# Optimization experiments

Measured on AMD Instinct MI355X. Metric: run time of the kernel, lower is better.

Reference implementation:

```python
import jax, jax.numpy as jnp
import numpy as np

N = 50000      # num_nodes
E = 800000     # num_edges (before self loops)
EMB = 128      # emb_dim
GH = 64        # gcn_hidden
TD = 4         # temporal_dim
B = 64         # batch of sequences
T = 200        # max sequence length
H = 128        # lstm_hidden (per direction)
IN_DIM = 2 + EMB + TD


def lstm_scan(x_tbi, w_ih, w_hh, b_ih, b_hh):
    """x_tbi: [T, B, I] -> hidden states [T, B, H]. PyTorch gate order i,f,g,o."""
    Bsz = x_tbi.shape[1]
    Hh = w_hh.shape[1]

    def step(carry, xt):
        h, c = carry
        g = xt @ w_ih.T + h @ w_hh.T + b_ih + b_hh
        i, f, gg, o = jnp.split(g, 4, axis=-1)
        c = jax.nn.sigmoid(f) * c + jax.nn.sigmoid(i) * jnp.tanh(gg)
        h = jax.nn.sigmoid(o) * jnp.tanh(c)
        return (h, c), h

    init = (jnp.zeros((Bsz, Hh), x_tbi.dtype), jnp.zeros((Bsz, Hh), x_tbi.dtype))
    _, hs = jax.lax.scan(step, init, x_tbi)
    return hs


def gcn_layer(x, W, b, src, dst, ew):
    """PyG GCNConv: linear -> symmetric-norm gather/scatter-add -> bias.
    (self loops already appended to src/dst/ew by caller)"""
    h = x @ W  # [N, out]
    deg = jax.ops.segment_sum(ew, dst, num_segments=N)
    dinv = jnp.where(deg > 0, jax.lax.rsqrt(deg), 0.0)
    norm = dinv[src] * ew * dinv[dst]            # [E+N]
    msg = h[src] * norm[:, None]                  # gather + scale
    return jax.ops.segment_sum(msg, dst, num_segments=N) + b


def setup_inputs() -> dict:
    key = jax.random.key(0)
    ks = jax.random.split(key, 16)
    s = 0.02
    return {
        'x_coords': jax.random.normal(ks[0], (N, 2), jnp.float32),
        'temporal_features': jax.random.uniform(ks[1], (N, TD), jnp.float32, -1.0, 1.0),
        'edge_index': jax.random.randint(ks[2], (2, E), 0, N),
        'edge_weight': jnp.ones((E,), jnp.float32),
        'seq': jax.random.randint(ks[3], (B, T), 0, N),
        'lengths': jax.random.randint(ks[4], (B,), 1, T + 1),
        'node_emb': jax.random.normal(ks[5], (N, EMB), jnp.float32) * s,
        'gcn1_w': jax.random.normal(ks[6], (IN_DIM, GH), jnp.float32) * s,
        'gcn1_b': jnp.zeros((GH,), jnp.float32),
        'gcn2_w': jax.random.normal(ks[7], (GH, EMB), jnp.float32) * s,
        'gcn2_b': jnp.zeros((EMB,), jnp.float32),
        'w_ih_f': jax.random.normal(ks[8], (4 * H, EMB), jnp.float32) * s,
        'w_hh_f': jax.random.normal(ks[9], (4 * H, H), jnp.float32) * s,
        'b_ih_f': jnp.zeros((4 * H,), jnp.float32),
        'b_hh_f': jnp.zeros((4 * H,), jnp.float32),
        'w_ih_b': jax.random.normal(ks[10], (4 * H, EMB), jnp.float32) * s,
        'w_hh_b': jax.random.normal(ks[11], (4 * H, H), jnp.float32) * s,
        'b_ih_b': jnp.zeros((4 * H,), jnp.float32),
        'b_hh_b': jnp.zeros((4 * H,), jnp.float32),
        'attn_w': jax.random.normal(ks[12], (2 * H,), jnp.float32) * s,
        'attn_b': jnp.zeros((), jnp.float32),
        'fc_w': jax.random.normal(ks[13], (2 * H, N), jnp.float32) * s,
        'fc_b': jnp.zeros((N,), jnp.float32),
    }


def reference(x_coords, temporal_features, edge_index, edge_weight, seq, lengths,
              node_emb, gcn1_w, gcn1_b, gcn2_w, gcn2_b,
              w_ih_f, w_hh_f, b_ih_f, b_hh_f,
              w_ih_b, w_hh_b, b_ih_b, b_hh_b,
              attn_w, attn_b, fc_w, fc_b):
    # --- GCN with self loops (PyG add_self_loops=True, fill_value=1) ---
    loop = jnp.arange(N)
    src = jnp.concatenate([edge_index[0], loop])
    dst = jnp.concatenate([edge_index[1], loop])
    ew = jnp.concatenate([edge_weight, jnp.ones((N,), edge_weight.dtype)])

    x = jnp.concatenate([x_coords, node_emb, temporal_features], axis=1)  # [N, 134]
    z = jax.nn.relu(gcn_layer(x, gcn1_w, gcn1_b, src, dst, ew))
    z = gcn_layer(z, gcn2_w, gcn2_b, src, dst, ew)  # dropout = identity (eval)

    # --- sequence embedding + BiLSTM ---
    seq_emb = z[seq]                                  # [B, T, EMB]
    h_f = lstm_scan(seq_emb.transpose(1, 0, 2), w_ih_f, w_hh_f, b_ih_f, b_hh_f)
    h_f = h_f.transpose(1, 0, 2)                      # [B, T, H]

    # backward direction: reverse each sequence within its valid length
    t = jnp.arange(T)
    valid = t[None, :] < lengths[:, None]             # [B, T]
    rev_idx = jnp.where(valid, lengths[:, None] - 1 - t[None, :], t[None, :])
    x_rev = jnp.take_along_axis(seq_emb, rev_idx[:, :, None], axis=1)
    h_b = lstm_scan(x_rev.transpose(1, 0, 2), w_ih_b, w_hh_b, b_ih_b, b_hh_b)
    h_b = jnp.take_along_axis(h_b.transpose(1, 0, 2), rev_idx[:, :, None], axis=1)

    lstm_out = jnp.concatenate([h_f, h_b], axis=-1)   # [B, T, 2H]

    # --- masked attention pooling ---
    scores = lstm_out @ attn_w + attn_b               # [B, T]
    scores = jnp.where(valid, scores, -jnp.inf)
    aw = jax.nn.softmax(scores, axis=1)
    context = jnp.einsum('bt,btd->bd', aw, lstm_out)  # [B, 2H]

    return context @ fc_w + fc_b                      # [B, N]
```

## Files before the change

### kernel.cpp

```cpp
#include <hip/hip_runtime.h>
#include <math.h>

#define NN 50000
#define NE 800000
#define EMB 128
#define GH 64
#define BB 64
#define TT 200
#define HH 128
#define G4 512
#define IND 134
#define PM 128
#define PO 128

__device__ __forceinline__ float sigf(float x) { return 1.0f / (1.0f + __expf(-x)); }
__device__ __forceinline__ float tanhf_(float x) { return 1.0f - 2.0f / (__expf(2.0f * x) + 1.0f); }
__device__ __forceinline__ void fma4(float4& a, float s, const float4 w) {
    a.x += s * w.x; a.y += s * w.y; a.z += s * w.z; a.w += s * w.w;
}

__global__ void hist_kernel(const int* __restrict__ ei, const float* __restrict__ ew,
                            int* __restrict__ cnt, float* __restrict__ degw) {
    int e = blockIdx.x * 256 + threadIdx.x;
    if (e >= NE) return;
    int d = ei[NE + e];
    atomicAdd(&cnt[d], 1);
    atomicAdd(&degw[d], ew[e]);
}

__global__ void dinv_kernel(const float* __restrict__ degw, float* __restrict__ dinv) {
    int n = blockIdx.x * 256 + threadIdx.x;
    if (n >= NN) return;
    dinv[n] = rsqrtf(degw[n] + 1.0f);
}

__global__ __launch_bounds__(1024) void scan1_kernel(const int* __restrict__ cnt,
                                                     int* __restrict__ rs, int* __restrict__ partials) {
    __shared__ int s[1024];
    int gid = blockIdx.x * 1024 + threadIdx.x;
    int v = (gid < NN) ? cnt[gid] : 0;
    s[threadIdx.x] = v;
    __syncthreads();
    for (int off = 1; off < 1024; off <<= 1) {
        int add = (threadIdx.x >= (unsigned)off) ? s[threadIdx.x - off] : 0;
        __syncthreads();
        s[threadIdx.x] += add;
        __syncthreads();
    }
    if (gid < NN) rs[gid] = s[threadIdx.x] - v;
    if (threadIdx.x == 1023) partials[blockIdx.x] = s[1023];
}

__global__ void scan2_kernel(int* __restrict__ partials, int nblk) {
    if (threadIdx.x == 0) {
        int acc = 0;
        for (int i = 0; i < nblk; ++i) { int v = partials[i]; partials[i] = acc; acc += v; }
    }
}

__global__ __launch_bounds__(1024) void scan3_kernel(const int* __restrict__ partials,
                                                     int* __restrict__ rs, int* __restrict__ cursor) {
    int gid = blockIdx.x * 1024 + threadIdx.x;
    if (gid < NN) {
        int v = rs[gid] + partials[gid >> 10];
        rs[gid] = v;
        cursor[gid] = v;
    }
    if (gid == 0) rs[NN] = NE;
}

__global__ void fill_kernel(const int* __restrict__ ei, const float* __restrict__ ew,
                            const float* __restrict__ dinv, int* __restrict__ cursor,
                            int* __restrict__ ssrc, float* __restrict__ sw) {
    int e = blockIdx.x * 256 + threadIdx.x;
    if (e >= NE) return;
    int s = ei[e], d = ei[NE + e];
    int pos = atomicAdd(&cursor[d], 1);
    ssrc[pos] = s;
    sw[pos] = ew[e] * dinv[s] * dinv[d];
}

__global__ __launch_bounds__(256) void gemm1_kernel(const float* __restrict__ coords,
                                                    const float* __restrict__ temporal,
                                                    const float* __restrict__ emb,
                                                    const float* __restrict__ W1,
                                                    float* __restrict__ h1) {
    __shared__ __align__(16) float wl[IND][GH];
    for (int i = threadIdx.x; i < IND * GH / 4; i += 256)
        ((float4*)wl)[i] = ((const float4*)W1)[i];
    __syncthreads();
    int n = blockIdx.x * 256 + threadIdx.x;
    if (n >= NN) return;
    float4 acc[16];
    float c0 = coords[2 * n], c1 = coords[2 * n + 1];
#pragma unroll
    for (int j = 0; j < 16; ++j) {
        float4 wa = *(const float4*)&wl[0][j * 4];
        float4 wb = *(const float4*)&wl[1][j * 4];
        float4 a;
        a.x = c0 * wa.x + c1 * wb.x; a.y = c0 * wa.y + c1 * wb.y;
        a.z = c0 * wa.z + c1 * wb.z; a.w = c0 * wa.w + c1 * wb.w;
        acc[j] = a;
    }
    const float4* er = (const float4*)(emb + (size_t)n * EMB);
#pragma unroll 2
    for (int k4 = 0; k4 < 32; ++k4) {
        float4 v = er[k4];
        int k = 2 + k4 * 4;
#pragma unroll
        for (int j = 0; j < 16; ++j) {
            fma4(acc[j], v.x, *(const float4*)&wl[k][j * 4]);
            fma4(acc[j], v.y, *(const float4*)&wl[k + 1][j * 4]);
            fma4(acc[j], v.z, *(const float4*)&wl[k + 2][j * 4]);
            fma4(acc[j], v.w, *(const float4*)&wl[k + 3][j * 4]);
        }
    }
    float t0 = temporal[4 * n], t1 = temporal[4 * n + 1], t2 = temporal[4 * n + 2], t3 = temporal[4 * n + 3];
#pragma unroll
    for (int j = 0; j < 16; ++j) {
        fma4(acc[j], t0, *(const float4*)&wl[130][j * 4]);
        fma4(acc[j], t1, *(const float4*)&wl[131][j * 4]);
        fma4(acc[j], t2, *(const float4*)&wl[132][j * 4]);
        fma4(acc[j], t3, *(const float4*)&wl[133][j * 4]);
        *(float4*)&h1[(size_t)n * GH + j * 4] = acc[j];
    }
}

__global__ __launch_bounds__(256) void agg_kernel(const float* __restrict__ hin,
                                                  const int* __restrict__ rs,
                                                  const int* __restrict__ ssrc,
                                                  const float* __restrict__ sw,
                                                  const float* __restrict__ dinv,
                                                  const float* __restrict__ bias, int relu,
                                                  float* __restrict__ hout) {
    int lane = threadIdx.x & 63;
    int wid = threadIdx.x >> 6;
    int n = blockIdx.x * 4 + wid;
    if (n >= NN) return;
    float dv = dinv[n];
    float acc = hin[(size_t)n * GH + lane] * (dv * dv);
    int i = rs[n], e1 = rs[n + 1];
    for (; i + 3 < e1; i += 4) {
        int s0 = ssrc[i], s1 = ssrc[i + 1], s2 = ssrc[i + 2], s3 = ssrc[i + 3];
        float w0 = sw[i], w1 = sw[i + 1], w2 = sw[i + 2], w3 = sw[i + 3];
        float a0 = hin[(size_t)s0 * GH + lane];
        float a1 = hin[(size_t)s1 * GH + lane];
        float a2 = hin[(size_t)s2 * GH + lane];
        float a3 = hin[(size_t)s3 * GH + lane];
        acc += a0 * w0 + a1 * w1 + a2 * w2 + a3 * w3;
    }
    for (; i < e1; ++i) acc += hin[(size_t)ssrc[i] * GH + lane] * sw[i];
    if (bias) acc += bias[lane];
    if (relu) acc = fmaxf(acc, 0.0f);
    hout[(size_t)n * GH + lane] = acc;
}

__global__ __launch_bounds__(256) void gemm2_kernel(const float* __restrict__ a2,
                                                    const float* __restrict__ W2,
                                                    const float* __restrict__ b2,
                                                    float* __restrict__ z2) {
    __shared__ __align__(16) float wl[GH][64];
    int j0 = blockIdx.y * 64;
    for (int i = threadIdx.x; i < GH * 16; i += 256) {
        int k = i >> 4, j4 = i & 15;
        *(float4*)&wl[k][j4 * 4] = *(const float4*)&W2[(size_t)k * EMB + j0 + j4 * 4];
    }
    __syncthreads();
    int n = blockIdx.x * 256 + threadIdx.x;
    if (n >= NN) return;
    float4 acc[16];
#pragma unroll
    for (int j = 0; j < 16; ++j) acc[j] = *(const float4*)&b2[j0 + j * 4];
    const float4* ar = (const float4*)(a2 + (size_t)n * GH);
#pragma unroll 2
    for (int k4 = 0; k4 < 16; ++k4) {
        float4 v = ar[k4];
        int k = k4 * 4;
#pragma unroll
        for (int j = 0; j < 16; ++j) {
            fma4(acc[j], v.x, *(const float4*)&wl[k][j * 4]);
            fma4(acc[j], v.y, *(const float4*)&wl[k + 1][j * 4]);
            fma4(acc[j], v.z, *(const float4*)&wl[k + 2][j * 4]);
            fma4(acc[j], v.w, *(const float4*)&wl[k + 3][j * 4]);
        }
    }
#pragma unroll
    for (int j = 0; j < 16; ++j)
        *(float4*)&z2[(size_t)n * EMB + j0 + j * 4] = acc[j];
}

__global__ void gather_kernel(const int* __restrict__ seq, const float* __restrict__ z2,
                              float* __restrict__ se) {
    int idx = blockIdx.x * 256 + threadIdx.x;
    if (idx >= BB * TT * 32) return;
    int r = idx >> 5, q = idx & 31;
    int node = seq[r];
    ((float4*)se)[(size_t)r * 32 + q] = ((const float4*)z2)[(size_t)node * 32 + q];
}

__global__ __launch_bounds__(256) void pregemm_kernel(const float* __restrict__ se,
                                                      const float* __restrict__ w_ih_f,
                                                      const float* __restrict__ w_ih_b,
                                                      const float* __restrict__ b_ih_f,
                                                      const float* __restrict__ b_hh_f,
                                                      const float* __restrict__ b_ih_b,
                                                      const float* __restrict__ b_hh_b,
                                                      const int* __restrict__ lengths,
                                                      float* __restrict__ xpf,
                                                      float* __restrict__ xpb) {
    int dir = blockIdx.z;
    const float* w_ih = dir ? w_ih_b : w_ih_f;
    int o0 = blockIdx.y * PO;
    int m0 = blockIdx.x * PM;
    __shared__ __align__(16) float xs[PM][EMB];
    __shared__ __align__(16) float ws[PO][EMB];
    __shared__ float bsh[PO];
    int tid = threadIdx.x;
#pragma unroll
    for (int i = 0; i < 16; ++i) {
        int idx = i * 256 + tid;
        int row = idx >> 5, c4 = idx & 31;
        float4 v = *(const float4*)&w_ih[(size_t)(o0 + row) * EMB + c4 * 4];
        *(float4*)&ws[row][(c4 ^ ((row >> 3) & 7)) * 4] = v;
    }
    if (tid < PO) bsh[tid] = dir ? (b_ih_b[o0 + tid] + b_hh_b[o0 + tid])
                                 : (b_ih_f[o0 + tid] + b_hh_f[o0 + tid]);
#pragma unroll
    for (int i = 0; i < 16; ++i) {
        int idx = i * 256 + tid;
        int r = idx >> 5, c4 = idx & 31;
        int m = m0 + r;
        int t = m >> 6, b = m & 63;
        int tsrc = t;
        if (dir) { int len = lengths[b]; tsrc = (t < len) ? (len - 1 - t) : t; }
        float4 v = *(const float4*)&se[((size_t)b * TT + tsrc) * EMB + c4 * 4];
        *(float4*)&xs[r][(c4 ^ ((r >> 3) & 3)) * 4] = v;
    }
    __syncthreads();
    int mt = tid >> 4, ot = tid & 15;
    int mswz = mt & 3, oswz = ot & 7;
    float acc[8][8];
#pragma unroll
    for (int mi = 0; mi < 8; ++mi)
#pragma unroll
        for (int oi = 0; oi < 8; ++oi) acc[mi][oi] = 0.0f;
    for (int k4 = 0; k4 < 32; ++k4) {
        int xk = (k4 ^ mswz) * 4;
        int wk = (k4 ^ oswz) * 4;
        float4 xv[8], wv[8];
#pragma unroll
        for (int mi = 0; mi < 8; ++mi) xv[mi] = *(const float4*)&xs[mt * 8 + mi][xk];
#pragma unroll
        for (int oi = 0; oi < 8; ++oi) wv[oi] = *(const float4*)&ws[ot * 8 + oi][wk];
#pragma unroll
        for (int mi = 0; mi < 8; ++mi)
#pragma unroll
            for (int oi = 0; oi < 8; ++oi)
                acc[mi][oi] += xv[mi].x * wv[oi].x + xv[mi].y * wv[oi].y
                             + xv[mi].z * wv[oi].z + xv[mi].w * wv[oi].w;
    }
    float* xp = dir ? xpb : xpf;
#pragma unroll
    for (int mi = 0; mi < 8; ++mi) {
        int m = m0 + mt * 8 + mi;
        int ob = ot * 8;
        float4 oa = make_float4(acc[mi][0] + bsh[ob + 0], acc[mi][1] + bsh[ob + 1],
                                acc[mi][2] + bsh[ob + 2], acc[mi][3] + bsh[ob + 3]);
        float4 obv = make_float4(acc[mi][4] + bsh[ob + 4], acc[mi][5] + bsh[ob + 5],
                                 acc[mi][6] + bsh[ob + 6], acc[mi][7] + bsh[ob + 7]);
        *(float4*)&xp[(size_t)m * G4 + o0 + ob] = oa;
        *(float4*)&xp[(size_t)m * G4 + o0 + ob + 4] = obv;
    }
}

__global__ __launch_bounds__(1024, 4) void lstm_kernel(const float* __restrict__ xpf,
                                                       const float* __restrict__ xpb,
                                                       const float* __restrict__ w_hh_f,
                                                       const float* __restrict__ w_hh_b,
                                                       const int* __restrict__ lengths,
                                                       float* __restrict__ hfo,
                                                       float* __restrict__ hbo) {
    int chain = blockIdx.x;
    int dir = chain & 1, b = chain >> 1;
    const float* w_hh = dir ? w_hh_b : w_hh_f;
    const float* xp = dir ? xpb : xpf;
    float* ho = dir ? hbo : hfo;
    int tid = threadIdx.x;
    int u = tid & 127;
    int kq = tid >> 7;
    int len = lengths[b];

    float4 W[4][4];
#pragma unroll
    for (int g = 0; g < 4; ++g)
#pragma unroll
        for (int j4 = 0; j4 < 4; ++j4)
            W[g][j4] = *(const float4*)&w_hh[(size_t)(g * HH + u) * HH + kq * 16 + j4 * 4];

    __shared__ __align__(16) float hl[HH];
    __shared__ __align__(16) float part[HH][9][4];
    if (tid < HH) hl[tid] = 0.0f;
    __syncthreads();

    float cst = 0.0f;
    float x0 = 0.f, x1 = 0.f, x2 = 0.f, x3 = 0.f;
    const float* xpt = xp + (size_t)b * G4 + u;
    if (tid < HH && len > 0) {
        x0 = xpt[0]; x1 = xpt[HH]; x2 = xpt[2 * HH]; x3 = xpt[3 * HH];
    }
    for (int t = 0; t < len; ++t) {
        const float4* h4 = (const float4*)&hl[kq * 16];
        float a0 = 0.f, a1 = 0.f, a2 = 0.f, a3 = 0.f;
#pragma unroll
        for (int j4 = 0; j4 < 4; ++j4) {
            float4 hv = h4[j4];
            a0 += W[0][j4].x * hv.x + W[0][j4].y * hv.y + W[0][j4].z * hv.z + W[0][j4].w * hv.w;
            a1 += W[1][j4].x * hv.x + W[1][j4].y * hv.y + W[1][j4].z * hv.z + W[1][j4].w * hv.w;
            a2 += W[2][j4].x * hv.x + W[2][j4].y * hv.y + W[2][j4].z * hv.z + W[2][j4].w * hv.w;
            a3 += W[3][j4].x * hv.x + W[3][j4].y * hv.y + W[3][j4].z * hv.z + W[3][j4].w * hv.w;
        }
        *(float4*)&part[u][kq][0] = make_float4(a0, a1, a2, a3);
        __syncthreads();
        if (tid < HH) {
            float n0 = 0.f, n1 = 0.f, n2 = 0.f, n3 = 0.f;
            if (t + 1 < len) {
                const float* xn = xpt + (size_t)(t + 1) * (BB * G4);
                n0 = xn[0]; n1 = xn[HH]; n2 = xn[2 * HH]; n3 = xn[3 * HH];
            }
            float s0 = x0, s1 = x1, s2 = x2, s3 = x3;
#pragma unroll
            for (int q = 0; q < 8; ++q) {
                float4 p = *(const float4*)&part[u][q][0];
                s0 += p.x; s1 += p.y; s2 += p.z; s3 += p.w;
            }
            float gi = sigf(s0), gf = sigf(s1), gg = tanhf_(s2), go = sigf(s3);
            cst = gf * cst + gi * gg;
            float h = go * tanhf_(cst);
            hl[u] = h;
            int tt = dir ? (len - 1 - t) : t;
            ho[((size_t)b * TT + tt) * HH + u] = h;
            x0 = n0; x1 = n1; x2 = n2; x3 = n3;
        }
        __syncthreads();
    }
}

__global__ __launch_bounds__(256) void attn_kernel(const float* __restrict__ hf,
                                                   const float* __restrict__ hb,
                                                   const float* __restrict__ attn_w,
                                                   const float* __restrict__ attn_b,
                                                   const int* __restrict__ lengths,
                                                   float* __restrict__ ctx) {
    int b = blockIdx.x;
    int tid = threadIdx.x;
    int len = lengths[b];
    __shared__ __align__(16) float wl[256];
    __shared__ float pl[256];
    __shared__ float red[256];
    wl[tid] = attn_w[tid];
    __syncthreads();
    float sc = -3.0e38f;
    if (tid < len) {
        const float4* rf = (const float4*)(hf + ((size_t)b * TT + tid) * HH);
        const float4* rb = (const float4*)(hb + ((size_t)b * TT + tid) * HH);
        const float4* w4 = (const float4*)wl;
        float s = attn_b[0];
        for (int k4 = 0; k4 < 32; ++k4) {
            float4 a = rf[k4], ww = w4[k4];
            s += a.x * ww.x + a.y * ww.y + a.z * ww.z + a.w * ww.w;
        }
        for (int k4 = 0; k4 < 32; ++k4) {
            float4 a = rb[k4], ww = w4[32 + k4];
            s += a.x * ww.x + a.y * ww.y + a.z * ww.z + a.w * ww.w;
        }
        sc = s;
    }
    red[tid] = sc;
    __syncthreads();
    for (int off = 128; off > 0; off >>= 1) {
        if (tid < off) red[tid] = fmaxf(red[tid], red[tid + off]);
        __syncthreads();
    }
    float mx = red[0];
    __syncthreads();
    float e = (tid < len) ? __expf(sc - mx) : 0.0f;
    red[tid] = e;
    __syncthreads();
    for (int off = 128; off > 0; off >>= 1) {
        if (tid < off) red[tid] += red[tid + off];
        __syncthreads();
    }
    float inv = 1.0f / red[0];
    pl[tid] = e * inv;
    __syncthreads();
    float acc = 0.0f;
    const float* basep = (tid < HH) ? (hf + (size_t)b * TT * HH + tid)
                                    : (hb + (size_t)b * TT * HH + (tid - HH));
#pragma unroll 4
    for (int t = 0; t < len; ++t) acc += pl[t] * basep[(size_t)t * HH];
    ctx[(size_t)b * 256 + tid] = acc;
}

__global__ __launch_bounds__(256) void fc_kernel(const float* __restrict__ ctx,
                                                 const float* __restrict__ fc_w,
                                                 const float* __restrict__ fc_b,
                                                 float* __restrict__ out) {
    __shared__ __align__(16) float cl[64][256];
    for (int i = threadIdx.x; i < 64 * 256 / 4; i += 256)
        ((float4*)cl)[i] = ((const float4*)ctx)[i];
    __syncthreads();
    int nb = threadIdx.x & 63;
    int bq = threadIdx.x >> 6;
    int n = blockIdx.x * 64 + nb;
    if (n >= NN) return;
    float acc[16];
#pragma unroll
    for (int i = 0; i < 16; ++i) acc[i] = 0.0f;
#pragma unroll 2
    for (int k4 = 0; k4 < 64; ++k4) {
        int k = k4 * 4;
        float w0 = fc_w[(size_t)k * NN + n];
        float w1 = fc_w[(size_t)(k + 1) * NN + n];
        float w2 = fc_w[(size_t)(k + 2) * NN + n];
        float w3 = fc_w[(size_t)(k + 3) * NN + n];
#pragma unroll
        for (int i = 0; i < 16; ++i) {
            float4 cv = *(const float4*)&cl[bq * 16 + i][k];
            acc[i] += cv.x * w0 + cv.y * w1 + cv.z * w2 + cv.w * w3;
        }
    }
    float fb = fc_b[n];
#pragma unroll
    for (int i = 0; i < 16; ++i)
        out[(size_t)(bq * 16 + i) * NN + n] = acc[i] + fb;
}

extern "C" void kernel_launch(void* const* d_in, const int* in_sizes, int n_in,
                              void* d_out, int out_size, void* d_ws, size_t ws_size,
                              hipStream_t stream) {
    const float* x_coords   = (const float*)d_in[0];
    const float* temporal   = (const float*)d_in[1];
    const int*   edge_index = (const int*)d_in[2];
    const float* edge_w     = (const float*)d_in[3];
    const int*   seq        = (const int*)d_in[4];
    const int*   lengths    = (const int*)d_in[5];
    const float* node_emb   = (const float*)d_in[6];
    const float* gcn1_w     = (const float*)d_in[7];
    const float* gcn1_b     = (const float*)d_in[8];
    const float* gcn2_w     = (const float*)d_in[9];
    const float* gcn2_b     = (const float*)d_in[10];
    const float* w_ih_f     = (const float*)d_in[11];
    const float* w_hh_f     = (const float*)d_in[12];
    const float* b_ih_f     = (const float*)d_in[13];
    const float* b_hh_f     = (const float*)d_in[14];
    const float* w_ih_b     = (const float*)d_in[15];
    const float* w_hh_b     = (const float*)d_in[16];
    const float* b_ih_b     = (const float*)d_in[17];
    const float* b_hh_b     = (const float*)d_in[18];
    const float* attn_w     = (const float*)d_in[19];
    const float* attn_b     = (const float*)d_in[20];
    const float* fc_w       = (const float*)d_in[21];
    const float* fc_b       = (const float*)d_in[22];
    float* out = (float*)d_out;

    char* base = (char*)d_ws;
    size_t off = 0;
    auto alloc = [&](size_t nbytes) -> void* {
        void* p = base + off;
        off = (off + nbytes + 255) & ~(size_t)255;
        return p;
    };
    int*   cnt     = (int*)alloc((size_t)2 * NN * 4);
    float* degw    = (float*)(cnt + NN);
    float* dinv    = (float*)alloc((size_t)NN * 4);
    int*   rs      = (int*)alloc(((size_t)NN + 1) * 4);
    int*   cursor  = (int*)alloc((size_t)NN * 4);
    int*   partials= (int*)alloc(64 * 4);
    int*   ssrc    = (int*)alloc((size_t)NE * 4);
    float* sw      = (float*)alloc((size_t)NE * 4);
    float* h1      = (float*)alloc((size_t)NN * GH * 4);
    float* z1      = (float*)alloc((size_t)NN * GH * 4);
    float* a2      = h1;
    float* z2      = (float*)alloc((size_t)NN * EMB * 4);
    float* se      = (float*)alloc((size_t)BB * TT * EMB * 4);
    float* xpf     = (float*)alloc((size_t)TT * BB * G4 * 4);
    float* xpb     = (float*)alloc((size_t)TT * BB * G4 * 4);
    float* hfo     = (float*)alloc((size_t)BB * TT * HH * 4);
    float* hbo     = (float*)alloc((size_t)BB * TT * HH * 4);
    float* ctx     = (float*)alloc((size_t)BB * 256 * 4);
    (void)ws_size; (void)in_sizes; (void)n_in; (void)out_size;

    hipMemsetAsync(cnt, 0, (size_t)2 * NN * 4, stream);

    hist_kernel<<<(NE + 255) / 256, 256, 0, stream>>>(edge_index, edge_w, cnt, degw);
    dinv_kernel<<<(NN + 255) / 256, 256, 0, stream>>>(degw, dinv);
    const int nblk = (NN + 1023) / 1024;
    scan1_kernel<<<nblk, 1024, 0, stream>>>(cnt, rs, partials);
    scan2_kernel<<<1, 64, 0, stream>>>(partials, nblk);
    scan3_kernel<<<nblk, 1024, 0, stream>>>(partials, rs, cursor);
    fill_kernel<<<(NE + 255) / 256, 256, 0, stream>>>(edge_index, edge_w, dinv, cursor, ssrc, sw);

    gemm1_kernel<<<(NN + 255) / 256, 256, 0, stream>>>(x_coords, temporal, node_emb, gcn1_w, h1);
    agg_kernel<<<(NN + 3) / 4, 256, 0, stream>>>(h1, rs, ssrc, sw, dinv, gcn1_b, 1, z1);
    agg_kernel<<<(NN + 3) / 4, 256, 0, stream>>>(z1, rs, ssrc, sw, dinv, (const float*)nullptr, 0, a2);
    gemm2_kernel<<<dim3((NN + 255) / 256, 2), 256, 0, stream>>>(a2, gcn2_w, gcn2_b, z2);

    gather_kernel<<<(BB * TT * 32 + 255) / 256, 256, 0, stream>>>(seq, z2, se);
    pregemm_kernel<<<dim3(TT * BB / PM, G4 / PO, 2), 256, 0, stream>>>(
        se, w_ih_f, w_ih_b, b_ih_f, b_hh_f, b_ih_b, b_hh_b, lengths, xpf, xpb);
    lstm_kernel<<<BB * 2, 1024, 0, stream>>>(xpf, xpb, w_hh_f, w_hh_b, lengths, hfo, hbo);
    attn_kernel<<<BB, 256, 0, stream>>>(hfo, hbo, attn_w, attn_b, lengths, ctx);
    fc_kernel<<<(NN + 63) / 64, 256, 0, stream>>>(ctx, fc_w, fc_b, out);
}
```

Before: 642.3 us.

## Use wave shuffles and double-buffered hidden state in LSTM; register-tile gemm2

The LSTM recurrence now places the 8 k-slices of each hidden unit in adjacent lanes of one wavefront and reduces the gate partials with xor shuffles. This replaces the shared partial array and one of two block barriers per timestep, and the hidden state is double-buffered in padded shared memory. Separately, the second GCN GEMM is rewritten as a 128x64 shared-memory tile with 4x8 register blocking and swizzled layout, using a pre-transposed weight from a new small kernel. Risks are shuffle overhead and one extra kernel launch.

```diff
diff --git a/kernel.cpp b/kernel.cpp
--- a/kernel.cpp
+++ b/kernel.cpp
@@ -155,38 +155,73 @@
     hout[(size_t)n * GH + lane] = acc;
 }
 
+__global__ void w2t_kernel(const float* __restrict__ W2, float* __restrict__ w2t) {
+    int i = blockIdx.x * 256 + threadIdx.x;
+    if (i >= GH * EMB) return;
+    int o = i >> 6, k = i & 63;
+    w2t[i] = W2[(size_t)k * EMB + o];
+}
+
 __global__ __launch_bounds__(256) void gemm2_kernel(const float* __restrict__ a2,
-                                                    const float* __restrict__ W2,
+                                                    const float* __restrict__ w2t,
                                                     const float* __restrict__ b2,
                                                     float* __restrict__ z2) {
-    __shared__ __align__(16) float wl[GH][64];
-    int j0 = blockIdx.y * 64;
-    for (int i = threadIdx.x; i < GH * 16; i += 256) {
-        int k = i >> 4, j4 = i & 15;
-        *(float4*)&wl[k][j4 * 4] = *(const float4*)&W2[(size_t)k * EMB + j0 + j4 * 4];
-    }
-    __syncthreads();
-    int n = blockIdx.x * 256 + threadIdx.x;
-    if (n >= NN) return;
-    float4 acc[16];
-#pragma unroll
-    for (int j = 0; j < 16; ++j) acc[j] = *(const float4*)&b2[j0 + j * 4];
-    const float4* ar = (const float4*)(a2 + (size_t)n * GH);
-#pragma unroll 2
+    int m0 = blockIdx.x * 128, o0 = blockIdx.y * 64;
+    __shared__ __align__(16) float xs[128][64];
+    __shared__ __align__(16) float wt[64][64];
+    __shared__ float bsh[64];
+    int tid = threadIdx.x;
+#pragma unroll
+    for (int i = 0; i < 8; ++i) {
+        int idx = i * 256 + tid;
+        int r = idx >> 4, c4 = idx & 15;
+        int m = m0 + r;
+        float4 v = (m < NN) ? *(const float4*)&a2[(size_t)m * GH + c4 * 4]
+                            : make_float4(0.f, 0.f, 0.f, 0.f);
+        *(float4*)&xs[r][(c4 ^ ((r >> 2) & 3)) * 4] = v;
+    }
+#pragma unroll
+    for (int i = 0; i < 4; ++i) {
+        int idx = i * 256 + tid;
+        int r = idx >> 4, c4 = idx & 15;
+        float4 v = *(const float4*)&w2t[(size_t)(o0 + r) * GH + c4 * 4];
+        *(float4*)&wt[r][(c4 ^ ((r >> 3) & 7)) * 4] = v;
+    }
+    if (tid < 64) bsh[tid] = b2[o0 + tid];
+    __syncthreads();
+    int mt = tid >> 3, ot = tid & 7;
+    float acc[4][8];
+#pragma unroll
+    for (int mi = 0; mi < 4; ++mi)
+#pragma unroll
+        for (int oi = 0; oi < 8; ++oi) acc[mi][oi] = 0.0f;
     for (int k4 = 0; k4 < 16; ++k4) {
-        float4 v = ar[k4];
-        int k = k4 * 4;
-#pragma unroll
-        for (int j = 0; j < 16; ++j) {
-            fma4(acc[j], v.x, *(const float4*)&wl[k][j * 4]);
-            fma4(acc[j], v.y, *(const float4*)&wl[k + 1][j * 4]);
-            fma4(acc[j], v.z, *(const float4*)&wl[k + 2][j * 4]);
-            fma4(acc[j], v.w, *(const float4*)&wl[k + 3][j * 4]);
-        }
-    }
-#pragma unroll
-    for (int j = 0; j < 16; ++j)
-        *(float4*)&z2[(size_t)n * EMB + j0 + j * 4] = acc[j];
+        int xc = (k4 ^ (mt & 3)) * 4;
+        int wc = (k4 ^ (ot & 7)) * 4;
+        float4 xv[4], wv[8];
+#pragma unroll
+        for (int mi = 0; mi < 4; ++mi) xv[mi] = *(const float4*)&xs[mt * 4 + mi][xc];
+#pragma unroll
+        for (int oi = 0; oi < 8; ++oi) wv[oi] = *(const float4*)&wt[ot * 8 + oi][wc];
+#pragma unroll
+        for (int mi = 0; mi < 4; ++mi)
+#pragma unroll
+            for (int oi = 0; oi < 8; ++oi)
+                acc[mi][oi] += xv[mi].x * wv[oi].x + xv[mi].y * wv[oi].y
+                             + xv[mi].z * wv[oi].z + xv[mi].w * wv[oi].w;
+    }
+#pragma unroll
+    for (int mi = 0; mi < 4; ++mi) {
+        int m = m0 + mt * 4 + mi;
+        if (m >= NN) continue;
+        int ob = ot * 8;
+        float4 oa = make_float4(acc[mi][0] + bsh[ob + 0], acc[mi][1] + bsh[ob + 1],
+                                acc[mi][2] + bsh[ob + 2], acc[mi][3] + bsh[ob + 3]);
+        float4 obv = make_float4(acc[mi][4] + bsh[ob + 4], acc[mi][5] + bsh[ob + 5],
+                                 acc[mi][6] + bsh[ob + 6], acc[mi][7] + bsh[ob + 7]);
+        *(float4*)&z2[(size_t)m * EMB + o0 + ob] = oa;
+        *(float4*)&z2[(size_t)m * EMB + o0 + ob + 4] = obv;
+    }
 }
 
 __global__ void gather_kernel(const int* __restrict__ seq, const float* __restrict__ z2,
@@ -286,8 +321,9 @@
     const float* xp = dir ? xpb : xpf;
     float* ho = dir ? hbo : hfo;
     int tid = threadIdx.x;
-    int u = tid & 127;
-    int kq = tid >> 7;
+    int wv = tid >> 6, lane = tid & 63;
+    int uu = lane >> 3, kq = lane & 7;
+    int u = wv * 8 + uu;
     int len = lengths[b];
 
     float4 W[4][4];
@@ -297,19 +333,17 @@
         for (int j4 = 0; j4 < 4; ++j4)
             W[g][j4] = *(const float4*)&w_hh[(size_t)(g * HH + u) * HH + kq * 16 + j4 * 4];
 
-    __shared__ __align__(16) float hl[HH];
-    __shared__ __align__(16) float part[HH][9][4];
-    if (tid < HH) hl[tid] = 0.0f;
-    __syncthreads();
-
+    __shared__ __align__(16) float hl[2][8][20];
+    if (tid < 320) ((float*)hl)[tid] = 0.0f;
+    __syncthreads();
+
+    bool act = (kq == 0);
+    const float* xb = xp + (size_t)b * G4 + u;
     float cst = 0.0f;
     float x0 = 0.f, x1 = 0.f, x2 = 0.f, x3 = 0.f;
-    const float* xpt = xp + (size_t)b * G4 + u;
-    if (tid < HH && len > 0) {
-        x0 = xpt[0]; x1 = xpt[HH]; x2 = xpt[2 * HH]; x3 = xpt[3 * HH];
-    }
+    if (act && len > 0) { x0 = xb[0]; x1 = xb[HH]; x2 = xb[2 * HH]; x3 = xb[3 * HH]; }
     for (int t = 0; t < len; ++t) {
-        const float4* h4 = (const float4*)&hl[kq * 16];
+        const float4* h4 = (const float4*)&hl[t & 1][kq][0];
         float a0 = 0.f, a1 = 0.f, a2 = 0.f, a3 = 0.f;
 #pragma unroll
         for (int j4 = 0; j4 < 4; ++j4) {
@@ -319,24 +353,24 @@
             a2 += W[2][j4].x * hv.x + W[2][j4].y * hv.y + W[2][j4].z * hv.z + W[2][j4].w * hv.w;
             a3 += W[3][j4].x * hv.x + W[3][j4].y * hv.y + W[3][j4].z * hv.z + W[3][j4].w * hv.w;
         }
-        *(float4*)&part[u][kq][0] = make_float4(a0, a1, a2, a3);
-        __syncthreads();
-        if (tid < HH) {
+#pragma unroll
+        for (int m = 1; m < 8; m <<= 1) {
+            a0 += __shfl_xor(a0, m, 64);
+            a1 += __shfl_xor(a1, m, 64);
+            a2 += __shfl_xor(a2, m, 64);
+            a3 += __shfl_xor(a3, m, 64);
+        }
+        if (act) {
             float n0 = 0.f, n1 = 0.f, n2 = 0.f, n3 = 0.f;
             if (t + 1 < len) {
-                const float* xn = xpt + (size_t)(t + 1) * (BB * G4);
+                const float* xn = xb + (size_t)(t + 1) * (BB * G4);
                 n0 = xn[0]; n1 = xn[HH]; n2 = xn[2 * HH]; n3 = xn[3 * HH];
             }
-            float s0 = x0, s1 = x1, s2 = x2, s3 = x3;
-#pragma unroll
-            for (int q = 0; q < 8; ++q) {
-                float4 p = *(const float4*)&part[u][q][0];
-                s0 += p.x; s1 += p.y; s2 += p.z; s3 += p.w;
-            }
-            float gi = sigf(s0), gf = sigf(s1), gg = tanhf_(s2), go = sigf(s3);
+            float gi = sigf(a0 + x0), gf = sigf(a1 + x1);
+            float gg = tanhf_(a2 + x2), go = sigf(a3 + x3);
             cst = gf * cst + gi * gg;
             float h = go * tanhf_(cst);
-            hl[u] = h;
+            hl[(t + 1) & 1][u >> 4][u & 15] = h;
             int tt = dir ? (len - 1 - t) : t;
             ho[((size_t)b * TT + tt) * HH + u] = h;
             x0 = n0; x1 = n1; x2 = n2; x3 = n3;
@@ -481,6 +515,7 @@
     float* h1      = (float*)alloc((size_t)NN * GH * 4);
     float* z1      = (float*)alloc((size_t)NN * GH * 4);
     float* a2      = h1;
+    float* w2t     = (float*)alloc((size_t)GH * EMB * 4);
     float* z2      = (float*)alloc((size_t)NN * EMB * 4);
     float* se      = (float*)alloc((size_t)BB * TT * EMB * 4);
     float* xpf     = (float*)alloc((size_t)TT * BB * G4 * 4);
@@ -499,11 +534,12 @@
     scan2_kernel<<<1, 64, 0, stream>>>(partials, nblk);
     scan3_kernel<<<nblk, 1024, 0, stream>>>(partials, rs, cursor);
     fill_kernel<<<(NE + 255) / 256, 256, 0, stream>>>(edge_index, edge_w, dinv, cursor, ssrc, sw);
+    w2t_kernel<<<(GH * EMB + 255) / 256, 256, 0, stream>>>(gcn2_w, w2t);
 
     gemm1_kernel<<<(NN + 255) / 256, 256, 0, stream>>>(x_coords, temporal, node_emb, gcn1_w, h1);
     agg_kernel<<<(NN + 3) / 4, 256, 0, stream>>>(h1, rs, ssrc, sw, dinv, gcn1_b, 1, z1);
     agg_kernel<<<(NN + 3) / 4, 256, 0, stream>>>(z1, rs, ssrc, sw, dinv, (const float*)nullptr, 0, a2);
-    gemm2_kernel<<<dim3((NN + 255) / 256, 2), 256, 0, stream>>>(a2, gcn2_w, gcn2_b, z2);
+    gemm2_kernel<<<dim3((NN + 127) / 128, 2), 256, 0, stream>>>(a2, w2t, gcn2_b, z2);
 
     gather_kernel<<<(BB * TT * 32 + 255) / 256, 256, 0, stream>>>(seq, z2, se);
     pregemm_kernel<<<dim3(TT * BB / PM, G4 / PO, 2), 256, 0, stream>>>(
```

New measurement: 701.0 us. +9.1%, slower.
